# Kernel optimization log

Measured on AMD Instinct MI355X. Metric: run time of the kernel, lower is better.

Reference implementation:

```python
import jax, jax.numpy as jnp
import numpy as np
import math

PS = 16            # patch size for SigmaPredictor
HID = 8            # hidden_dim
SCALE = HID ** -0.5
SIGMA_CAP = 6.0    # BoundedSoftplus threshold
EPS_S = 1e-6       # BoundedSoftplus eps


def setup_inputs() -> dict:
    key = jax.random.key(0)
    ks = jax.random.split(key, 10)
    B, C, H, W = 2, 1, 384, 384
    d_in = C * PS * PS  # 256
    r = lambda k_, sh: jax.random.normal(k_, sh, dtype=jnp.float32) * 0.1
    z = lambda sh: jnp.zeros(sh, dtype=jnp.float32)
    return {
        "x": jax.random.uniform(ks[0], (B, C, H, W), dtype=jnp.float32),
        "Wq": r(ks[1], (d_in, HID)), "bq": z((HID,)),
        "Wk": r(ks[2], (d_in, HID)), "bk": z((HID,)),
        "Wv": r(ks[3], (d_in, HID)), "bv": z((HID,)),
        "Wsq": r(ks[4], (HID, HID)), "bsq": z((HID,)),
        "Wsk": r(ks[5], (HID, HID)), "bsk": z((HID,)),
        "Wsv": r(ks[6], (HID, HID)), "bsv": z((HID,)),
        "ln_g": jnp.ones((HID,), jnp.float32), "ln_b": z((HID,)),
        "Wp": r(ks[7], (HID, 3)),
        # bias ~4 -> sigmas ~4 -> kernel size k=13 (production-scale support)
        "bp": jnp.full((3,), 4.0, dtype=jnp.float32),
    }


def _attn(q, k, v):
    a = jax.nn.softmax(jnp.einsum('bnd,bmd->bnm', q, k) * SCALE, axis=-1)
    return jnp.einsum('bnm,bmd->bnd', a, v)


def _predict_sigmas(x, Wq, bq, Wk, bk, Wv, bv, Wsq, bsq, Wsk, bsk, Wsv, bsv, ln_g, ln_b, Wp, bp):
    b, c, h, w = x.shape
    Hp, Wn = h // PS, w // PS
    # unfold into non-overlapping patches: [B, Hp*Wn, C*PS*PS]
    pat = x.reshape(b, c, Hp, PS, Wn, PS).transpose(0, 2, 4, 1, 3, 5).reshape(b, Hp * Wn, c * PS * PS)
    feats = _attn(pat @ Wq + bq, pat @ Wk + bk, pat @ Wv + bv)
    o = _attn(feats @ Wsq + bsq, feats @ Wsk + bsk, feats @ Wsv + bsv)
    mu = o.mean(-1, keepdims=True)
    var = ((o - mu) ** 2).mean(-1, keepdims=True)
    o = (o - mu) / jnp.sqrt(var + 1e-5) * ln_g + ln_b
    s = jnp.minimum(jax.nn.softplus(o @ Wp + bp), SIGMA_CAP) + EPS_S  # BoundedSoftplus
    s = s.reshape(b, Hp, Wn, 3)
    # nearest-neighbor upsample to full resolution: [B, H, W, 3]
    return jnp.repeat(jnp.repeat(s, PS, axis=1), PS, axis=2)


def _bilateral(x, s, k):
    b, c, h, w = x.shape
    sx, sy, sr = s[..., 0], s[..., 1], s[..., 2]
    half = k // 2
    xp = jnp.pad(x, ((0, 0), (0, 0), (half, half), (half, half)))
    # [B, C, H, W, k*k], dy-major to match torch unfold/meshgrid ordering
    patches = jnp.stack([xp[:, :, dy:dy + h, dx:dx + w]
                         for dy in range(k) for dx in range(k)], axis=-1)
    coords = jnp.arange(-half, half + 1, dtype=jnp.float32)
    yy, xx = jnp.meshgrid(coords, coords, indexing='ij')
    xx2 = (xx ** 2).reshape(-1)
    yy2 = (yy ** 2).reshape(-1)
    # spatial kernel [B, H, W, k*k]
    sp = jnp.exp(-xx2 / (2 * sx[..., None] ** 2) - yy2 / (2 * sy[..., None] ** 2))
    # range kernel (C == 1 branch) [B, C, H, W, k*k]
    rg = jnp.exp(-(x[..., None] - patches) ** 2 / (2 * sr[:, None, :, :, None] ** 2))
    comb = sp[:, None] * rg
    norm = comb / (comb.sum(-1, keepdims=True) + 1e-8)
    return (patches * norm).sum(-1)


def reference(x, Wq, bq, Wk, bk, Wv, bv, Wsq, bsq, Wsk, bsk, Wsv, bsv, ln_g, ln_b, Wp, bp):
    s = _predict_sigmas(x, Wq, bq, Wk, bk, Wv, bv, Wsq, bsq, Wsk, bsk, Wsv, bsv, ln_g, ln_b, Wp, bp)
    # data-dependent kernel size, computed eagerly (matches torch .item())
    m = float(jnp.maximum(s[..., 0].max(), s[..., 1].max()))
    k = int(2 * math.ceil(m + 1))
    if k % 2 == 0:
        k += 1
    return _bilateral(x, s, k)
```

## Files before the change

kernel.cpp:

```cpp
#include <hip/hip_runtime.h>

#define N_TOK 576
#define HP    24
#define PS    16
#define IMG   384
#define ATTN_SCALE 0.35355339059327373f
#define NBLK  576
#define BAR_STRIDE 132

__device__ __forceinline__ void stg_u32(float* p, float v) {
    union { float f; unsigned u; } c; c.f = v;
    __hip_atomic_store((unsigned*)p, c.u, __ATOMIC_RELAXED,
                       __HIP_MEMORY_SCOPE_AGENT);
}
__device__ __forceinline__ float2 ldg_f2(const float* p) {
    unsigned long long u = __hip_atomic_load(
        (const unsigned long long*)p, __ATOMIC_RELAXED,
        __HIP_MEMORY_SCOPE_AGENT);
    union { unsigned long long u; float2 f; } c; c.u = u; return c.f;
}
__device__ __forceinline__ void ldrow8(const float* p, float r[8]) {
    const float2 a = ldg_f2(p),   b = ldg_f2(p+2);
    const float2 c = ldg_f2(p+4), d = ldg_f2(p+6);
    r[0]=a.x; r[1]=a.y; r[2]=b.x; r[3]=b.y;
    r[4]=c.x; r[5]=c.y; r[6]=d.x; r[7]=d.y;
}

__device__ __forceinline__ void gbar(unsigned* base)
{
    __syncthreads();
    if (threadIdx.x == 0) {
        unsigned* grp  = base + (blockIdx.x & 7) * 16;
        unsigned* root = base + 128;
        unsigned* flag = base + 129;
        const unsigned old = __hip_atomic_fetch_add(
            grp, 1u, __ATOMIC_RELAXED, __HIP_MEMORY_SCOPE_AGENT);
        if (old == (NBLK/8) - 1u) {
            const unsigned r = __hip_atomic_fetch_add(
                root, 1u, __ATOMIC_RELAXED, __HIP_MEMORY_SCOPE_AGENT);
            if (r == 7u)
                __hip_atomic_store(flag, 1u, __ATOMIC_RELAXED,
                                   __HIP_MEMORY_SCOPE_AGENT);
        }
        while (!__hip_atomic_load(flag, __ATOMIC_RELAXED,
                                  __HIP_MEMORY_SCOPE_AGENT))
            __builtin_amdgcn_s_sleep(8);
    }
    __syncthreads();
}

__global__ __launch_bounds__(256, 3) void k_all(
    const float* __restrict__ x,
    const float* __restrict__ Wq, const float* __restrict__ bq,
    const float* __restrict__ Wk, const float* __restrict__ bk,
    const float* __restrict__ Wv, const float* __restrict__ bv,
    const float* __restrict__ Wsq, const float* __restrict__ bsq,
    const float* __restrict__ Wsk, const float* __restrict__ bsk,
    const float* __restrict__ Wsv, const float* __restrict__ bsv,
    const float* __restrict__ ln_g, const float* __restrict__ ln_b,
    const float* __restrict__ Wp,   const float* __restrict__ bp,
    float* __restrict__ k1, float* __restrict__ v1,
    float* __restrict__ k2, float* __restrict__ v2,
    unsigned* __restrict__ ctl,
    float* __restrict__ out)
{
    __shared__ float tile[2][32*40];
    __shared__ float spt[2][17*17];
    __shared__ float s_sig[2][3];
    __shared__ int   s_half;

    const int t = threadIdx.x, lane = t & 63, w = t >> 6;
    const int blk = blockIdx.x;
    unsigned* smax = ctl + 3*BAR_STRIDE;

    float qv[8];
    if (w < 2) {
        const int p  = blk*2 + w;
        const int b  = p / N_TOK, n = p % N_TOK;
        const int py = n / HP, px = n % HP;
        const int iy = lane >> 2, ix0 = (lane & 3) * 4;
        const float4 pv = *(const float4*)
            &x[b*IMG*IMG + (py*PS + iy)*IMG + px*PS + ix0];

        float acc[24];
#pragma unroll
        for (int j = 0; j < 24; ++j) acc[j] = 0.f;
#pragma unroll
        for (int j = 0; j < 4; ++j) {
            const int ft = 4*lane + j;
            const float pvj = ((const float*)&pv)[j];
#pragma unroll
            for (int h = 0; h < 8; ++h) {
                acc[h]      += pvj * Wq[ft*8 + h];
                acc[8 + h]  += pvj * Wk[ft*8 + h];
                acc[16 + h] += pvj * Wv[ft*8 + h];
            }
        }
#pragma unroll
        for (int off = 32; off; off >>= 1)
#pragma unroll
            for (int j = 0; j < 24; ++j) acc[j] += __shfl_xor(acc[j], off);

#pragma unroll
        for (int h = 0; h < 8; ++h) qv[h] = acc[h] + bq[h];
        if (lane >= 8 && lane < 16)
            stg_u32(&k1[p*8 + (lane & 7)], acc[8 + (lane & 7)]  + bk[lane & 7]);
        if (lane >= 16 && lane < 24)
            stg_u32(&v1[p*8 + (lane & 7)], acc[16 + (lane & 7)] + bv[lane & 7]);
    } else {
        const int i  = w - 2;
        const int p  = blk*2 + i;
        const int b  = p / N_TOK, n = p % N_TOK;
        const int py = n / HP, px = n % HP;
        const float* xb = x + b*IMG*IMG;
        float* tl = tile[i];
#pragma unroll
        for (int j = 0; j < 16; ++j) {
            const int e  = j*64 + lane;
            const int yy = e >> 5, xx = e & 31;
            const int gy = py*PS + yy - 8, gx = px*PS + xx - 8;
            float v = 0.f;
            if ((unsigned)gy < IMG && (unsigned)gx < IMG)
                v = xb[gy*IMG + gx];
            tl[yy*40 + xx] = v;
        }
    }
    gbar(ctl + 0*BAR_STRIDE);

    float qv2[8];
    if (w < 2) {
        const int tok = blk*2 + w;
        const int b   = tok / N_TOK;
        const float* kbp = k1 + b*N_TOK*8;
        const float* vbp = v1 + b*N_TOK*8;

        float sc[9], mx = -1e30f;
#pragma unroll
        for (int ch = 0; ch < 9; ++ch) {
            float kr[8]; ldrow8(kbp + (ch*64 + lane)*8, kr);
            float d = 0.f;
#pragma unroll
            for (int h = 0; h < 8; ++h) d += qv[h]*kr[h];
            sc[ch] = d * ATTN_SCALE;
            mx = fmaxf(mx, sc[ch]);
        }
#pragma unroll
        for (int off = 32; off; off >>= 1) mx = fmaxf(mx, __shfl_xor(mx, off));

        float ssum = 0.f, o[8];
#pragma unroll
        for (int h = 0; h < 8; ++h) o[h] = 0.f;
#pragma unroll
        for (int ch = 0; ch < 9; ++ch) {
            float vr[8]; ldrow8(vbp + (ch*64 + lane)*8, vr);
            const float pw = __expf(sc[ch] - mx);
            ssum += pw;
#pragma unroll
            for (int h = 0; h < 8; ++h) o[h] += pw*vr[h];
        }
#pragma unroll
        for (int off = 32; off; off >>= 1) {
            ssum += __shfl_xor(ssum, off);
#pragma unroll
            for (int h = 0; h < 8; ++h) o[h] += __shfl_xor(o[h], off);
        }
        const float inv = 1.f/ssum;
        float f[8];
#pragma unroll
        for (int h = 0; h < 8; ++h) f[h] = o[h]*inv;

        float sproj = 0.f;
        if (lane < 24) {
            const int mat = lane >> 3, h = lane & 7;
            const float* Wm = (mat==0)?Wsq:(mat==1)?Wsk:Wsv;
            const float* bm = (mat==0)?bsq:(mat==1)?bsk:bsv;
            float s = bm[h];
#pragma unroll
            for (int j = 0; j < 8; ++j) s += f[j]*Wm[j*8 + h];
            sproj = s;
            if (mat == 1) stg_u32(&k2[tok*8 + h], s);
            if (mat == 2) stg_u32(&v2[tok*8 + h], s);
        }
#pragma unroll
        for (int h = 0; h < 8; ++h) qv2[h] = __shfl(sproj, h);
    }
    gbar(ctl + 1*BAR_STRIDE);

    if (w < 2) {
        const int tok = blk*2 + w;
        const int b   = tok / N_TOK;
        const float* kbp = k2 + b*N_TOK*8;
        const float* vbp = v2 + b*N_TOK*8;

        float sc[9], mx = -1e30f;
#pragma unroll
        for (int ch = 0; ch < 9; ++ch) {
            float kr[8]; ldrow8(kbp + (ch*64 + lane)*8, kr);
            float d = 0.f;
#pragma unroll
            for (int h = 0; h < 8; ++h) d += qv2[h]*kr[h];
            sc[ch] = d * ATTN_SCALE;
            mx = fmaxf(mx, sc[ch]);
        }
#pragma unroll
        for (int off = 32; off; off >>= 1) mx = fmaxf(mx, __shfl_xor(mx, off));

        float ssum = 0.f, o[8];
#pragma unroll
        for (int h = 0; h < 8; ++h) o[h] = 0.f;
#pragma unroll
        for (int ch = 0; ch < 9; ++ch) {
            float vr[8]; ldrow8(vbp + (ch*64 + lane)*8, vr);
            const float pw = __expf(sc[ch] - mx);
            ssum += pw;
#pragma unroll
            for (int h = 0; h < 8; ++h) o[h] += pw*vr[h];
        }
#pragma unroll
        for (int off = 32; off; off >>= 1) {
            ssum += __shfl_xor(ssum, off);
#pragma unroll
            for (int h = 0; h < 8; ++h) o[h] += __shfl_xor(o[h], off);
        }

        if (lane == 0) {
            const float inv = 1.f/ssum;
            float f[8];
            float mu = 0.f;
#pragma unroll
            for (int h = 0; h < 8; ++h) { f[h] = o[h]*inv; mu += f[h]; }
            mu *= 0.125f;
            float var = 0.f;
#pragma unroll
            for (int h = 0; h < 8; ++h) { const float d = f[h]-mu; var += d*d; }
            var *= 0.125f;
            const float rinv = rsqrtf(var + 1e-5f);
            float on[8];
#pragma unroll
            for (int h = 0; h < 8; ++h)
                on[h] = (f[h]-mu)*rinv*ln_g[h] + ln_b[h];
            float sv[3];
#pragma unroll
            for (int c = 0; c < 3; ++c) {
                float z = bp[c];
#pragma unroll
                for (int j = 0; j < 8; ++j) z += on[j]*Wp[j*3 + c];
                const float sp = (z > 20.f) ? z : log1pf(__expf(z));
                sv[c] = fminf(sp, 6.0f) + 1e-6f;
                s_sig[w][c] = sv[c];
            }
            atomicMax((int*)smax, __float_as_int(fmaxf(sv[0], sv[1])));
        }
    }
    gbar(ctl + 2*BAR_STRIDE);

    if (t == 0) {
        const int mi = __hip_atomic_load((const int*)smax, __ATOMIC_RELAXED,
                                         __HIP_MEMORY_SCOPE_AGENT);
        const float m = __int_as_float(mi);
        int h = (int)ceilf(m + 1.0f);
        if (h < 1) h = 1;
        if (h > 8) h = 8;
        s_half = h;
    }
    __syncthreads();
    const int half = s_half;
    const int k    = 2*half + 1;
    const int kk   = k*k;
    const int off0 = 8 - half;
    const int tx = t & 15, ty = t >> 4;

    for (int ii = t; ii < 2*kk; ii += 256) {
        const int i = (ii >= kk) ? 1 : 0;
        const int e = ii - (i ? kk : 0);
        const int dy = e / k, dx = e - dy*k;
        const float fy = (float)(dy - half), fx = (float)(dx - half);
        const float axc = -0.5f/(s_sig[i][0]*s_sig[i][0]);
        const float ayc = -0.5f/(s_sig[i][1]*s_sig[i][1]);
        spt[i][e] = __expf(ayc*fy*fy + axc*fx*fx);
    }
    __syncthreads();

#pragma unroll
    for (int i = 0; i < 2; ++i) {
        const int p  = blk*2 + i;
        const int b  = p / N_TOK, n = p % N_TOK;
        const int py = n / HP, px = n % HP;
        const float sr  = s_sig[i][2];
        const float ar2 = -0.72134752044448170f/(sr*sr);
        const float* tl = tile[i];
        const float c   = tl[(ty+8)*40 + (tx+8)];

        float num = 0.f, den = 0.f;
        for (int dy = 0; dy < k; ++dy) {
            const float* row = &tl[(ty+dy+off0)*40 + tx + off0];
            const float* spr = &spt[i][dy*k];
            for (int dx = 0; dx < k; ++dx) {
                const float pix = row[dx];
                const float d   = c - pix;
                const float wgt = spr[dx] * exp2f(ar2*d*d);
                den += wgt;
                num += wgt*pix;
            }
        }
        out[b*IMG*IMG + (py*PS + ty)*IMG + (px*PS + tx)] = num/(den + 1e-8f);
    }
}

extern "C" void kernel_launch(void* const* d_in, const int* in_sizes, int n_in,
                              void* d_out, int out_size, void* d_ws, size_t ws_size,
                              hipStream_t stream)
{
    const float* x    = (const float*)d_in[0];
    const float* Wq   = (const float*)d_in[1];
    const float* bq   = (const float*)d_in[2];
    const float* Wk   = (const float*)d_in[3];
    const float* bk   = (const float*)d_in[4];
    const float* Wv   = (const float*)d_in[5];
    const float* bv   = (const float*)d_in[6];
    const float* Wsq  = (const float*)d_in[7];
    const float* bsq  = (const float*)d_in[8];
    const float* Wsk  = (const float*)d_in[9];
    const float* bsk  = (const float*)d_in[10];
    const float* Wsv  = (const float*)d_in[11];
    const float* bsv  = (const float*)d_in[12];
    const float* ln_g = (const float*)d_in[13];
    const float* ln_b = (const float*)d_in[14];
    const float* Wp   = (const float*)d_in[15];
    const float* bp   = (const float*)d_in[16];

    float* W  = (float*)d_ws;
    float* k1 = W;
    float* v1 = W +  9216;
    float* k2 = W + 18432;
    float* v2 = W + 27648;
    unsigned* ctl = (unsigned*)(W + 36864);

    hipMemsetAsync(ctl, 0, (3*BAR_STRIDE + 1)*sizeof(unsigned), stream);

    k_all<<<NBLK, 256, 0, stream>>>(x, Wq, bq, Wk, bk, Wv, bv,
                                    Wsq, bsq, Wsk, bsk, Wsv, bsv,
                                    ln_g, ln_b, Wp, bp,
                                    k1, v1, k2, v2, ctl, (float*)d_out);
}
```

Baseline: 161.0 us.

## Use four tokens per block with all waves computing, stage K/V in LDS

Halves the block count so each of the four waves handles its own token in the projection and attention stages, instead of two waves idling while the other two load the image tile. The per-batch K and V rows are staged cooperatively into shared memory, transposed, after each grid barrier, rather than being read redundantly from global memory by every wave. The bilateral tile is loaded after the sigma stage, sized to the actual kernel half-width, and processed sequentially for four patches with a reused tile. This cuts global traffic and barrier participants, but adds serial patch loops, extra block-wide syncs and a large LDS footprint that lowers occupancy.

```diff
diff --git a/kernel.cpp b/kernel.cpp
--- a/kernel.cpp
+++ b/kernel.cpp
@@ -5,7 +5,7 @@
 #define PS    16
 #define IMG   384
 #define ATTN_SCALE 0.35355339059327373f
-#define NBLK  576
+#define NBLK  288
 #define BAR_STRIDE 132
 
 __device__ __forceinline__ void stg_u32(float* p, float v) {
@@ -18,12 +18,6 @@
         (const unsigned long long*)p, __ATOMIC_RELAXED,
         __HIP_MEMORY_SCOPE_AGENT);
     union { unsigned long long u; float2 f; } c; c.u = u; return c.f;
-}
-__device__ __forceinline__ void ldrow8(const float* p, float r[8]) {
-    const float2 a = ldg_f2(p),   b = ldg_f2(p+2);
-    const float2 c = ldg_f2(p+4), d = ldg_f2(p+6);
-    r[0]=a.x; r[1]=a.y; r[2]=b.x; r[3]=b.y;
-    r[4]=c.x; r[5]=c.y; r[6]=d.x; r[7]=d.y;
 }
 
 __device__ __forceinline__ void gbar(unsigned* base)
@@ -44,12 +38,12 @@
         }
         while (!__hip_atomic_load(flag, __ATOMIC_RELAXED,
                                   __HIP_MEMORY_SCOPE_AGENT))
-            __builtin_amdgcn_s_sleep(8);
-    }
-    __syncthreads();
-}
-
-__global__ __launch_bounds__(256, 3) void k_all(
+            __builtin_amdgcn_s_sleep(2);
+    }
+    __syncthreads();
+}
+
+__global__ __launch_bounds__(256, 2) void k_all(
     const float* __restrict__ x,
     const float* __restrict__ Wq, const float* __restrict__ bq,
     const float* __restrict__ Wk, const float* __restrict__ bk,
@@ -64,19 +58,21 @@
     unsigned* __restrict__ ctl,
     float* __restrict__ out)
 {
-    __shared__ float tile[2][32*40];
-    __shared__ float spt[2][17*17];
-    __shared__ float s_sig[2][3];
+    __shared__ float kv[16][578];
+    __shared__ float tile[32*40];
+    __shared__ float spt[17*17];
+    __shared__ float s_sig[4][3];
     __shared__ int   s_half;
 
     const int t = threadIdx.x, lane = t & 63, w = t >> 6;
     const int blk = blockIdx.x;
+    const int tok = blk*4 + w;
+    const int b   = tok / N_TOK;
     unsigned* smax = ctl + 3*BAR_STRIDE;
 
     float qv[8];
-    if (w < 2) {
-        const int p  = blk*2 + w;
-        const int b  = p / N_TOK, n = p % N_TOK;
+    {
+        const int n  = tok % N_TOK;
         const int py = n / HP, px = n % HP;
         const int iy = lane >> 2, ix0 = (lane & 3) * 4;
         const float4 pv = *(const float4*)
@@ -104,43 +100,37 @@
 #pragma unroll
         for (int h = 0; h < 8; ++h) qv[h] = acc[h] + bq[h];
         if (lane >= 8 && lane < 16)
-            stg_u32(&k1[p*8 + (lane & 7)], acc[8 + (lane & 7)]  + bk[lane & 7]);
+            stg_u32(&k1[tok*8 + (lane & 7)], acc[8 + (lane & 7)]  + bk[lane & 7]);
         if (lane >= 16 && lane < 24)
-            stg_u32(&v1[p*8 + (lane & 7)], acc[16 + (lane & 7)] + bv[lane & 7]);
-    } else {
-        const int i  = w - 2;
-        const int p  = blk*2 + i;
-        const int b  = p / N_TOK, n = p % N_TOK;
-        const int py = n / HP, px = n % HP;
-        const float* xb = x + b*IMG*IMG;
-        float* tl = tile[i];
-#pragma unroll
-        for (int j = 0; j < 16; ++j) {
-            const int e  = j*64 + lane;
-            const int yy = e >> 5, xx = e & 31;
-            const int gy = py*PS + yy - 8, gx = px*PS + xx - 8;
-            float v = 0.f;
-            if ((unsigned)gy < IMG && (unsigned)gx < IMG)
-                v = xb[gy*IMG + gx];
-            tl[yy*40 + xx] = v;
-        }
+            stg_u32(&v1[tok*8 + (lane & 7)], acc[16 + (lane & 7)] + bv[lane & 7]);
     }
     gbar(ctl + 0*BAR_STRIDE);
 
+    {
+        const float* kb = k1 + b*N_TOK*8;
+        const float* vb = v1 + b*N_TOK*8;
+#pragma unroll
+        for (int j = 0; j < 18; ++j) {
+            const int e   = t + j*256;
+            const int src = (e >= 2304) ? 1 : 0;
+            const int idx = src ? e - 2304 : e;
+            const int r = idx >> 2, hp = idx & 3;
+            const float2 d = ldg_f2((src ? vb : kb) + r*8 + hp*2);
+            kv[src*8 + 2*hp + 0][r] = d.x;
+            kv[src*8 + 2*hp + 1][r] = d.y;
+        }
+    }
+    __syncthreads();
+
     float qv2[8];
-    if (w < 2) {
-        const int tok = blk*2 + w;
-        const int b   = tok / N_TOK;
-        const float* kbp = k1 + b*N_TOK*8;
-        const float* vbp = v1 + b*N_TOK*8;
-
+    {
         float sc[9], mx = -1e30f;
 #pragma unroll
         for (int ch = 0; ch < 9; ++ch) {
-            float kr[8]; ldrow8(kbp + (ch*64 + lane)*8, kr);
+            const int r = ch*64 + lane;
             float d = 0.f;
 #pragma unroll
-            for (int h = 0; h < 8; ++h) d += qv[h]*kr[h];
+            for (int h = 0; h < 8; ++h) d += qv[h]*kv[h][r];
             sc[ch] = d * ATTN_SCALE;
             mx = fmaxf(mx, sc[ch]);
         }
@@ -152,11 +142,11 @@
         for (int h = 0; h < 8; ++h) o[h] = 0.f;
 #pragma unroll
         for (int ch = 0; ch < 9; ++ch) {
-            float vr[8]; ldrow8(vbp + (ch*64 + lane)*8, vr);
+            const int r = ch*64 + lane;
             const float pw = __expf(sc[ch] - mx);
             ssum += pw;
 #pragma unroll
-            for (int h = 0; h < 8; ++h) o[h] += pw*vr[h];
+            for (int h = 0; h < 8; ++h) o[h] += pw*kv[8 + h][r];
         }
 #pragma unroll
         for (int off = 32; off; off >>= 1) {
@@ -186,19 +176,30 @@
     }
     gbar(ctl + 1*BAR_STRIDE);
 
-    if (w < 2) {
-        const int tok = blk*2 + w;
-        const int b   = tok / N_TOK;
-        const float* kbp = k2 + b*N_TOK*8;
-        const float* vbp = v2 + b*N_TOK*8;
-
+    {
+        const float* kb = k2 + b*N_TOK*8;
+        const float* vb = v2 + b*N_TOK*8;
+#pragma unroll
+        for (int j = 0; j < 18; ++j) {
+            const int e   = t + j*256;
+            const int src = (e >= 2304) ? 1 : 0;
+            const int idx = src ? e - 2304 : e;
+            const int r = idx >> 2, hp = idx & 3;
+            const float2 d = ldg_f2((src ? vb : kb) + r*8 + hp*2);
+            kv[src*8 + 2*hp + 0][r] = d.x;
+            kv[src*8 + 2*hp + 1][r] = d.y;
+        }
+    }
+    __syncthreads();
+
+    {
         float sc[9], mx = -1e30f;
 #pragma unroll
         for (int ch = 0; ch < 9; ++ch) {
-            float kr[8]; ldrow8(kbp + (ch*64 + lane)*8, kr);
+            const int r = ch*64 + lane;
             float d = 0.f;
 #pragma unroll
-            for (int h = 0; h < 8; ++h) d += qv2[h]*kr[h];
+            for (int h = 0; h < 8; ++h) d += qv2[h]*kv[h][r];
             sc[ch] = d * ATTN_SCALE;
             mx = fmaxf(mx, sc[ch]);
         }
@@ -210,11 +211,11 @@
         for (int h = 0; h < 8; ++h) o[h] = 0.f;
 #pragma unroll
         for (int ch = 0; ch < 9; ++ch) {
-            float vr[8]; ldrow8(vbp + (ch*64 + lane)*8, vr);
+            const int r = ch*64 + lane;
             const float pw = __expf(sc[ch] - mx);
             ssum += pw;
 #pragma unroll
-            for (int h = 0; h < 8; ++h) o[h] += pw*vr[h];
+            for (int h = 0; h < 8; ++h) o[h] += pw*kv[8 + h][r];
         }
 #pragma unroll
         for (int off = 32; off; off >>= 1) {
@@ -264,37 +265,45 @@
         s_half = h;
     }
     __syncthreads();
-    const int half = s_half;
-    const int k    = 2*half + 1;
-    const int kk   = k*k;
-    const int off0 = 8 - half;
+    const int half  = s_half;
+    const int k     = 2*half + 1;
+    const int tilew = PS + 2*half;
     const int tx = t & 15, ty = t >> 4;
 
-    for (int ii = t; ii < 2*kk; ii += 256) {
-        const int i = (ii >= kk) ? 1 : 0;
-        const int e = ii - (i ? kk : 0);
-        const int dy = e / k, dx = e - dy*k;
-        const float fy = (float)(dy - half), fx = (float)(dx - half);
-        const float axc = -0.5f/(s_sig[i][0]*s_sig[i][0]);
-        const float ayc = -0.5f/(s_sig[i][1]*s_sig[i][1]);
-        spt[i][e] = __expf(ayc*fy*fy + axc*fx*fx);
-    }
-    __syncthreads();
-
-#pragma unroll
-    for (int i = 0; i < 2; ++i) {
-        const int p  = blk*2 + i;
-        const int b  = p / N_TOK, n = p % N_TOK;
+    for (int i = 0; i < 4; ++i) {
+        const int p  = blk*4 + i;
+        const int bb = p / N_TOK, n = p % N_TOK;
         const int py = n / HP, px = n % HP;
-        const float sr  = s_sig[i][2];
+        const float sx = s_sig[i][0], sy = s_sig[i][1], sr = s_sig[i][2];
+        const float* xb = x + bb*IMG*IMG;
+
+        for (int yy = ty; yy < tilew; yy += 16) {
+            const int gy = py*PS + yy - half;
+            for (int xx = tx; xx < tilew; xx += 16) {
+                const int gx = px*PS + xx - half;
+                float v = 0.f;
+                if ((unsigned)gy < IMG && (unsigned)gx < IMG)
+                    v = xb[gy*IMG + gx];
+                tile[yy*40 + xx] = v;
+            }
+        }
+        {
+            const float axc = -0.5f/(sx*sx);
+            const float ayc = -0.5f/(sy*sy);
+            for (int ii = t; ii < k*k; ii += 256) {
+                const int dy = ii / k, dx = ii - dy*k;
+                const float fy = (float)(dy - half), fx = (float)(dx - half);
+                spt[ii] = __expf(ayc*fy*fy + axc*fx*fx);
+            }
+        }
+        __syncthreads();
+
+        const float c   = tile[(ty+half)*40 + (tx+half)];
         const float ar2 = -0.72134752044448170f/(sr*sr);
-        const float* tl = tile[i];
-        const float c   = tl[(ty+8)*40 + (tx+8)];
-
         float num = 0.f, den = 0.f;
         for (int dy = 0; dy < k; ++dy) {
-            const float* row = &tl[(ty+dy+off0)*40 + tx + off0];
-            const float* spr = &spt[i][dy*k];
+            const float* row = &tile[(ty+dy)*40 + tx];
+            const float* spr = &spt[dy*k];
             for (int dx = 0; dx < k; ++dx) {
                 const float pix = row[dx];
                 const float d   = c - pix;
@@ -303,7 +312,8 @@
                 num += wgt*pix;
             }
         }
-        out[b*IMG*IMG + (py*PS + ty)*IMG + (px*PS + tx)] = num/(den + 1e-8f);
+        out[bb*IMG*IMG + (py*PS + ty)*IMG + (px*PS + tx)] = num/(den + 1e-8f);
+        __syncthreads();
     }
 }
 
```

Measured after the change: 180.1 us. 11.8% more time.
